# Kernel optimization log

Hardware: AMD Instinct MI355X
Metric: run time of the kernel (lower is better)

Reference implementation:

```python
import jax, jax.numpy as jnp
import numpy as np

H, N, D, K = 4, 512, 64, 64  # n_heads, node_num, d_model, sparse_k
TEMP = 0.5
EPS = 1e-10


def setup_inputs() -> dict:
    key = jax.random.key(0)
    k1, k2, k3 = jax.random.split(key, 3)
    feats = jax.random.normal(k1, (H, N, D), jnp.float32)
    # torch Linear init ~ U(-1/sqrt(fan_in), 1/sqrt(fan_in)); Gaussian scale is fine for a baseline
    W_out = jax.random.normal(k2, (2 * D, D), jnp.float32) * (1.0 / np.sqrt(2 * D))
    b_out = jnp.zeros((D,), jnp.float32)
    W_cat = jax.random.normal(k3, (D, 2), jnp.float32) * (1.0 / np.sqrt(D))
    b_cat = jnp.zeros((2,), jnp.float32)
    return {"feats": feats, "W_out": W_out, "b_out": b_out,
            "W_cat": W_cat, "b_cat": b_cat, "sparse_k": K}


def reference(feats, W_out, b_out, W_cat, b_cat, sparse_k):
    H_, N_, D_ = feats.shape
    E = N_ * N_
    e = jnp.arange(E)
    rec_idx = e // N_   # receiver node of edge e (rel_rec one-hot gather)
    snd_idx = e % N_    # sender node of edge e (rel_send one-hot gather)
    # cat([senders, receivers], -1): [H, E, 2D]
    x = jnp.concatenate([feats[:, snd_idx], feats[:, rec_idx]], axis=-1)
    h = jax.nn.relu(x @ W_out + b_out)          # [H, E, D]
    logits = h @ W_cat + b_cat                  # [H, E, 2]
    # gumbel-softmax, hard (straight-through)
    U = jax.random.uniform(jax.random.key(42), logits.shape, jnp.float32)
    g = -jnp.log(-jnp.log(U + EPS) + EPS)
    y_soft = jax.nn.softmax((logits + g) / TEMP, axis=-1)
    y_hard = jax.nn.one_hot(jnp.argmax(y_soft, axis=-1), 2, dtype=y_soft.dtype)
    y = jax.lax.stop_gradient(y_hard - y_soft) + y_soft
    connection_matrix = y[..., 1].reshape(H_, N_, N_)
    connection_prob = jax.nn.softmax(logits, axis=-1)[..., 1]  # [H, E]
    _, top_idx = jax.lax.top_k(connection_prob, sparse_k)      # top-k over edges per head
    sparse_labels = jnp.zeros_like(connection_prob).at[
        jnp.arange(H_)[:, None], top_idx].set(1.0)
    return connection_matrix, connection_prob, sparse_labels
```

## Files before the change

kernel.cpp:

```cpp
#include <hip/hip_runtime.h>
#include <stdint.h>

#define H_ 4
#define N_ 512
#define D_ 64
#define E_ (N_ * N_)
#define HE_ (H_ * E_)
#define EPS_ 1e-10f

__device__ __forceinline__ void tf2x32(unsigned x0, unsigned x1,
                                       unsigned& o0, unsigned& o1) {
  const unsigned ks0 = 0u;
  const unsigned ks1 = 42u;
  const unsigned ks2 = 0x1BD11BDAu ^ ks0 ^ ks1;
  x0 += ks0; x1 += ks1;
#define TFR(r) { x0 += x1; x1 = (x1 << (r)) | (x1 >> (32 - (r))); x1 ^= x0; }
  TFR(13) TFR(15) TFR(26) TFR(6)
  x0 += ks1; x1 += ks2 + 1u;
  TFR(17) TFR(29) TFR(16) TFR(24)
  x0 += ks2; x1 += ks0 + 2u;
  TFR(13) TFR(15) TFR(26) TFR(6)
  x0 += ks0; x1 += ks1 + 3u;
  TFR(17) TFR(29) TFR(16) TFR(24)
  x0 += ks1; x1 += ks2 + 4u;
  TFR(13) TFR(15) TFR(26) TFR(6)
  x0 += ks2; x1 += ks0 + 5u;
#undef TFR
  o0 = x0; o1 = x1;
}

__device__ __forceinline__ unsigned rng_bits(unsigned j) {
  unsigned a, b;
  tf2x32(0u, j, a, b);
  return a ^ b;
}

__device__ __forceinline__ float u01(unsigned bits) {
  return __uint_as_float((bits >> 9) | 0x3f800000u) - 1.0f;
}

__global__ __launch_bounds__(256) void precompute_ab(
    const float* __restrict__ feats, const float* __restrict__ W_out,
    float* __restrict__ A, float* __restrict__ B,
    unsigned* __restrict__ cnt, unsigned* __restrict__ done) {
  int row = blockIdx.x * 4 + (threadIdx.x >> 6);
  int d = threadIdx.x & 63;
  if (blockIdx.x == 0) {
    if (threadIdx.x < 4) cnt[threadIdx.x] = 0u;
    else if (threadIdx.x < 8) done[threadIdx.x - 4] = 0u;
  }
  __shared__ float f[4][64];
  f[threadIdx.x >> 6][d] = feats[row * D_ + d];
  __syncthreads();
  const float* fr = f[threadIdx.x >> 6];
  float a = 0.f, b = 0.f;
#pragma unroll 8
  for (int k = 0; k < D_; ++k) {
    float fv = fr[k];
    a = fmaf(fv, W_out[k * D_ + d], a);
    b = fmaf(fv, W_out[(k + D_) * D_ + d], b);
  }
  A[row * D_ + d] = a;
  B[row * D_ + d] = b;
}

__global__ __launch_bounds__(256, 4) void edge_kernel(
    const float* __restrict__ A, const float* __restrict__ B,
    const float* __restrict__ b_out, const float* __restrict__ W_cat,
    const float* __restrict__ b_cat, float* __restrict__ out,
    unsigned long long* __restrict__ blockmax) {
  __shared__ __align__(16) float Ash[64][68];
  __shared__ __align__(16) float Bsh[16][64];
  __shared__ float4 bsh4[16];
  __shared__ float4 wc4[32];
  __shared__ float bc2[2];
  __shared__ unsigned long long wmax[4];

  const int t = threadIdx.x;
  const int h = blockIdx.z;
  const int snd_base = blockIdx.x * 64;
  const int rec_base = blockIdx.y * 16;

  {
    const float4* A4 = (const float4*)(A + (h * N_ + snd_base) * D_);
    for (int i = t; i < 1024; i += 256)
      *(float4*)&Ash[i >> 4][(i & 15) << 2] = A4[i];
    const float4* B4 = (const float4*)(B + (h * N_ + rec_base) * D_);
    *(float4*)&Bsh[t >> 4][(t & 15) << 2] = B4[t];
  }
  if (t < 16) bsh4[t] = ((const float4*)b_out)[t];
  else if (t < 48) wc4[t - 16] = ((const float4*)W_cat)[t - 16];
  else if (t == 48) { bc2[0] = b_cat[0]; bc2[1] = b_cat[1]; }
  __syncthreads();

  const int s = t & 63;
  const int rg = (t >> 6) * 4;

  float l0[4], l1[4];
#pragma unroll
  for (int r = 0; r < 4; ++r) { l0[r] = 0.f; l1[r] = 0.f; }

#pragma unroll
  for (int d4 = 0; d4 < 16; ++d4) {
    const float4 a0 = *(const float4*)&Ash[s][d4 << 2];
    const float4 bd = bsh4[d4];
    const float4 wA = wc4[2 * d4];
    const float4 wB = wc4[2 * d4 + 1];
#pragma unroll
    for (int r = 0; r < 4; ++r) {
      const float4 bv = *(const float4*)&Bsh[rg + r][d4 << 2];
      float t0;
      t0 = fmaxf((a0.x + bv.x) + bd.x, 0.f);
      l0[r] = fmaf(t0, wA.x, l0[r]); l1[r] = fmaf(t0, wA.y, l1[r]);
      t0 = fmaxf((a0.y + bv.y) + bd.y, 0.f);
      l0[r] = fmaf(t0, wA.z, l0[r]); l1[r] = fmaf(t0, wA.w, l1[r]);
      t0 = fmaxf((a0.z + bv.z) + bd.z, 0.f);
      l0[r] = fmaf(t0, wB.x, l0[r]); l1[r] = fmaf(t0, wB.y, l1[r]);
      t0 = fmaxf((a0.w + bv.w) + bd.w, 0.f);
      l0[r] = fmaf(t0, wB.z, l0[r]); l1[r] = fmaf(t0, wB.w, l1[r]);
    }
  }

  unsigned long long mk = 0ull;
#pragma unroll
  for (int r = 0; r < 4; ++r) {
    float L0 = l0[r] + bc2[0];
    float L1 = l1[r] + bc2[1];
    const unsigned snd = (unsigned)(snd_base + s);
    const unsigned rec = (unsigned)(rec_base + rg + r);
    const unsigned e = rec * (unsigned)N_ + snd;
    const unsigned base = ((unsigned)h << 18) + e;
    const unsigned j0 = base * 2u;

    float uu0 = u01(rng_bits(j0));
    float uu1 = u01(rng_bits(j0 + 1u));
    float g0 = -logf(-logf(uu0 + EPS_) + EPS_);
    float g1 = -logf(-logf(uu1 + EPS_) + EPS_);

    float cm = ((L1 + g1) > (L0 + g0)) ? 1.0f : 0.0f;

    float lm = fmaxf(L0, L1);
    float p0 = expf(L0 - lm), p1 = expf(L1 - lm);
    float pr = p1 / (p0 + p1);

    out[base] = cm;
    out[HE_ + base] = pr;
    out[2 * HE_ + base] = 0.f;

    unsigned long long key =
        ((unsigned long long)__float_as_uint(pr) << 32) | (unsigned)(~e);
    mk = key > mk ? key : mk;
  }

#pragma unroll
  for (int off = 32; off; off >>= 1) {
    unsigned long long o = __shfl_xor(mk, off, 64);
    mk = o > mk ? o : mk;
  }
  if ((t & 63) == 0) wmax[t >> 6] = mk;
  __syncthreads();
  if (t == 0) {
    unsigned long long m = wmax[0];
#pragma unroll
    for (int i = 1; i < 4; ++i) m = wmax[i] > m ? wmax[i] : m;
    blockmax[h * 256 + blockIdx.y * gridDim.x + blockIdx.x] = m;
  }
}

__global__ __launch_bounds__(512) void topk_fused(
    const float* __restrict__ prob, const unsigned long long* __restrict__ blockmax,
    unsigned* __restrict__ cnt, unsigned* __restrict__ done,
    unsigned long long* __restrict__ cand, float* __restrict__ sparse) {
  __shared__ unsigned long long keys[512];
  __shared__ unsigned long long thrS;
  __shared__ unsigned tkS;
  const int t = threadIdx.x, h = blockIdx.y, blk = blockIdx.x;

  if (t < 256) keys[t] = blockmax[h * 256 + t];
  __syncthreads();
  if (t < 256) {
    unsigned long long my = keys[t];
    int rank = 0;
    for (int j = 0; j < 256; ++j) rank += (keys[j] > my);
    if (rank == 63) thrS = my;
  }
  __syncthreads();
  const unsigned long long thr = thrS;

  const unsigned seg = (unsigned)blk * 4096u;
#pragma unroll
  for (int i = 0; i < 2; ++i) {
    const unsigned e0 = seg + (unsigned)i * 2048u + (unsigned)t * 4u;
    float4 p = *(const float4*)(prob + (unsigned)h * E_ + e0);
    float pv[4] = {p.x, p.y, p.z, p.w};
#pragma unroll
    for (int k2 = 0; k2 < 4; ++k2) {
      unsigned e = e0 + (unsigned)k2;
      unsigned long long key =
          ((unsigned long long)__float_as_uint(pv[k2]) << 32) | (unsigned)(~e);
      if (key >= thr) {
        unsigned pos = atomicAdd(&cnt[h], 1u);
        if (pos < 512u) cand[h * 512 + pos] = key;
      }
    }
  }
  __syncthreads();
  if (t == 0) { __threadfence(); tkS = atomicAdd(&done[h], 1u); }
  __syncthreads();

  if (tkS == 63u) {
    if (t == 0) __threadfence();
    __syncthreads();
    unsigned n = atomicAdd(&cnt[h], 0u);
    if (n > 512u) n = 512u;
    keys[t] = (t < (int)n) ? cand[h * 512 + t] : 0ull;
    __syncthreads();
    for (int k = 2; k <= 512; k <<= 1)
      for (int j = k >> 1; j > 0; j >>= 1) {
        int ixj = t ^ j;
        if (ixj > t) {
          unsigned long long a = keys[t], b = keys[ixj];
          bool up = (t & k) == 0;
          if ((a > b) == up) { keys[t] = b; keys[ixj] = a; }
        }
        __syncthreads();
      }
    if (t >= 448) {
      unsigned e = ~(unsigned)(keys[t] & 0xFFFFFFFFull);
      if (e < (unsigned)E_) sparse[(unsigned)h * E_ + e] = 1.0f;
    }
  }
}

extern "C" void kernel_launch(void* const* d_in, const int* in_sizes, int n_in,
                              void* d_out, int out_size, void* d_ws, size_t ws_size,
                              hipStream_t stream) {
  const float* feats = (const float*)d_in[0];
  const float* W_out = (const float*)d_in[1];
  const float* b_out = (const float*)d_in[2];
  const float* W_cat = (const float*)d_in[3];
  const float* b_cat = (const float*)d_in[4];
  float* out = (float*)d_out;

  float* A = (float*)d_ws;
  float* B = A + H_ * N_ * D_;
  unsigned long long* blockmax = (unsigned long long*)(B + H_ * N_ * D_);
  unsigned long long* cand = blockmax + H_ * 256;
  unsigned* cnt = (unsigned*)(cand + H_ * 512);
  unsigned* done = cnt + H_;

  precompute_ab<<<dim3(H_ * N_ / 4), dim3(256), 0, stream>>>(feats, W_out, A, B,
                                                             cnt, done);
  edge_kernel<<<dim3(N_ / 64, N_ / 16, H_), dim3(256), 0, stream>>>(
      A, B, b_out, W_cat, b_cat, out, blockmax);
  topk_fused<<<dim3(64, H_), dim3(512), 0, stream>>>(out + HE_, blockmax, cnt,
                                                     done, cand, out + 2 * HE_);
}
```

Measured before the change: 107.8 us.

## Fuse top-k selection into edge kernel using a grid-wide spin barrier

Merges the edge and top-k kernels into one launch. Each block publishes its max key, spins on a per-head atomic counter until all 256 blocks of that head have arrived, computes the threshold, and pushes its register-held candidate keys directly. This avoids re-reading the probability array and one kernel launch. The sparse-label zeros are also written as float4 stores. The spin barrier assumes all 1024 blocks are co-resident (256 threads, up to 4 blocks per SIMD-bound launch); if they are not, it can deadlock.

```diff
diff --git a/kernel.cpp b/kernel.cpp
--- a/kernel.cpp
+++ b/kernel.cpp
@@ -41,14 +41,10 @@
 
 __global__ __launch_bounds__(256) void precompute_ab(
     const float* __restrict__ feats, const float* __restrict__ W_out,
-    float* __restrict__ A, float* __restrict__ B,
-    unsigned* __restrict__ cnt, unsigned* __restrict__ done) {
+    float* __restrict__ A, float* __restrict__ B, unsigned* __restrict__ ctrl) {
   int row = blockIdx.x * 4 + (threadIdx.x >> 6);
   int d = threadIdx.x & 63;
-  if (blockIdx.x == 0) {
-    if (threadIdx.x < 4) cnt[threadIdx.x] = 0u;
-    else if (threadIdx.x < 8) done[threadIdx.x - 4] = 0u;
-  }
+  if (blockIdx.x == 0 && threadIdx.x < 12) ctrl[threadIdx.x] = 0u;
   __shared__ float f[4][64];
   f[threadIdx.x >> 6][d] = feats[row * D_ + d];
   __syncthreads();
@@ -64,22 +60,29 @@
   B[row * D_ + d] = b;
 }
 
-__global__ __launch_bounds__(256, 4) void edge_kernel(
+__global__ __launch_bounds__(256, 4) void edge_topk(
     const float* __restrict__ A, const float* __restrict__ B,
     const float* __restrict__ b_out, const float* __restrict__ W_cat,
     const float* __restrict__ b_cat, float* __restrict__ out,
-    unsigned long long* __restrict__ blockmax) {
+    unsigned long long* __restrict__ blockmax,
+    unsigned long long* __restrict__ cand, unsigned* __restrict__ ctrl) {
   __shared__ __align__(16) float Ash[64][68];
   __shared__ __align__(16) float Bsh[16][64];
   __shared__ float4 bsh4[16];
   __shared__ float4 wc4[32];
   __shared__ float bc2[2];
   __shared__ unsigned long long wmax[4];
+  __shared__ unsigned long long sortk[512];
+  __shared__ unsigned long long thrS;
 
   const int t = threadIdx.x;
   const int h = blockIdx.z;
   const int snd_base = blockIdx.x * 64;
   const int rec_base = blockIdx.y * 16;
+  const int bm_idx = blockIdx.y * 8 + blockIdx.x;
+  unsigned* cnt = ctrl;
+  unsigned* done0 = ctrl + 4;
+  unsigned* done1 = ctrl + 8;
 
   {
     const float4* A4 = (const float4*)(A + (h * N_ + snd_base) * D_);
@@ -121,6 +124,7 @@
     }
   }
 
+  unsigned long long ekey[4];
   unsigned long long mk = 0ull;
 #pragma unroll
   for (int r = 0; r < 4; ++r) {
@@ -145,11 +149,18 @@
 
     out[base] = cm;
     out[HE_ + base] = pr;
-    out[2 * HE_ + base] = 0.f;
 
     unsigned long long key =
         ((unsigned long long)__float_as_uint(pr) << 32) | (unsigned)(~e);
+    ekey[r] = key;
     mk = key > mk ? key : mk;
+  }
+
+  {
+    const float4 z4 = {0.f, 0.f, 0.f, 0.f};
+    *(float4*)&out[2u * HE_ + ((unsigned)h << 18) +
+                   (unsigned)(rec_base + (t >> 4)) * N_ + (unsigned)snd_base +
+                   ((unsigned)(t & 15) << 2)] = z4;
   }
 
 #pragma unroll
@@ -160,74 +171,66 @@
   if ((t & 63) == 0) wmax[t >> 6] = mk;
   __syncthreads();
   if (t == 0) {
-    unsigned long long m = wmax[0];
-#pragma unroll
-    for (int i = 1; i < 4; ++i) m = wmax[i] > m ? wmax[i] : m;
-    blockmax[h * 256 + blockIdx.y * gridDim.x + blockIdx.x] = m;
-  }
-}
-
-__global__ __launch_bounds__(512) void topk_fused(
-    const float* __restrict__ prob, const unsigned long long* __restrict__ blockmax,
-    unsigned* __restrict__ cnt, unsigned* __restrict__ done,
-    unsigned long long* __restrict__ cand, float* __restrict__ sparse) {
-  __shared__ unsigned long long keys[512];
-  __shared__ unsigned long long thrS;
-  __shared__ unsigned tkS;
-  const int t = threadIdx.x, h = blockIdx.y, blk = blockIdx.x;
-
-  if (t < 256) keys[t] = blockmax[h * 256 + t];
-  __syncthreads();
-  if (t < 256) {
-    unsigned long long my = keys[t];
+    unsigned long long mx = wmax[0];
+#pragma unroll
+    for (int i = 1; i < 4; ++i) mx = wmax[i] > mx ? wmax[i] : mx;
+    blockmax[h * 256 + bm_idx] = mx;
+    __threadfence();
+    atomicAdd(&done0[h], 1u);
+    while (atomicAdd(&done0[h], 0u) < 256u) __builtin_amdgcn_s_sleep(2);
+    __threadfence();
+  }
+  __syncthreads();
+
+  sortk[t] = blockmax[h * 256 + t];
+  __syncthreads();
+  {
+    unsigned long long my = sortk[t];
     int rank = 0;
-    for (int j = 0; j < 256; ++j) rank += (keys[j] > my);
+    for (int j = 0; j < 256; ++j) rank += (sortk[j] > my);
     if (rank == 63) thrS = my;
   }
   __syncthreads();
   const unsigned long long thr = thrS;
 
-  const unsigned seg = (unsigned)blk * 4096u;
-#pragma unroll
-  for (int i = 0; i < 2; ++i) {
-    const unsigned e0 = seg + (unsigned)i * 2048u + (unsigned)t * 4u;
-    float4 p = *(const float4*)(prob + (unsigned)h * E_ + e0);
-    float pv[4] = {p.x, p.y, p.z, p.w};
-#pragma unroll
-    for (int k2 = 0; k2 < 4; ++k2) {
-      unsigned e = e0 + (unsigned)k2;
-      unsigned long long key =
-          ((unsigned long long)__float_as_uint(pv[k2]) << 32) | (unsigned)(~e);
-      if (key >= thr) {
-        unsigned pos = atomicAdd(&cnt[h], 1u);
-        if (pos < 512u) cand[h * 512 + pos] = key;
-      }
-    }
-  }
-  __syncthreads();
-  if (t == 0) { __threadfence(); tkS = atomicAdd(&done[h], 1u); }
-  __syncthreads();
-
-  if (tkS == 63u) {
-    if (t == 0) __threadfence();
+#pragma unroll
+  for (int r = 0; r < 4; ++r) {
+    if (ekey[r] >= thr) {
+      unsigned pos = atomicAdd(&cnt[h], 1u);
+      if (pos < 512u) cand[h * 512 + pos] = ekey[r];
+    }
+  }
+  __syncthreads();
+  if (t == 0) { __threadfence(); atomicAdd(&done1[h], 1u); }
+
+  if (bm_idx == 0) {
+    if (t == 0) {
+      while (atomicAdd(&done1[h], 0u) < 256u) __builtin_amdgcn_s_sleep(2);
+      __threadfence();
+    }
     __syncthreads();
     unsigned n = atomicAdd(&cnt[h], 0u);
     if (n > 512u) n = 512u;
-    keys[t] = (t < (int)n) ? cand[h * 512 + t] : 0ull;
+    sortk[t] = (t < (int)n) ? cand[h * 512 + t] : 0ull;
+    sortk[t + 256] = (t + 256 < (int)n) ? cand[h * 512 + t + 256] : 0ull;
     __syncthreads();
     for (int k = 2; k <= 512; k <<= 1)
       for (int j = k >> 1; j > 0; j >>= 1) {
-        int ixj = t ^ j;
-        if (ixj > t) {
-          unsigned long long a = keys[t], b = keys[ixj];
-          bool up = (t & k) == 0;
-          if ((a > b) == up) { keys[t] = b; keys[ixj] = a; }
+#pragma unroll
+        for (int half = 0; half < 2; ++half) {
+          int idx = t + half * 256;
+          int ixj = idx ^ j;
+          if (ixj > idx) {
+            unsigned long long x = sortk[idx], y = sortk[ixj];
+            bool up = (idx & k) == 0;
+            if ((x > y) == up) { sortk[idx] = y; sortk[ixj] = x; }
+          }
         }
         __syncthreads();
       }
-    if (t >= 448) {
-      unsigned e = ~(unsigned)(keys[t] & 0xFFFFFFFFull);
-      if (e < (unsigned)E_) sparse[(unsigned)h * E_ + e] = 1.0f;
+    if (t >= 192) {
+      unsigned e = ~(unsigned)(sortk[t + 256] & 0xFFFFFFFFull);
+      if (e < (unsigned)E_) out[2u * HE_ + ((unsigned)h << 18) + e] = 1.0f;
     }
   }
 }
@@ -246,13 +249,10 @@
   float* B = A + H_ * N_ * D_;
   unsigned long long* blockmax = (unsigned long long*)(B + H_ * N_ * D_);
   unsigned long long* cand = blockmax + H_ * 256;
-  unsigned* cnt = (unsigned*)(cand + H_ * 512);
-  unsigned* done = cnt + H_;
+  unsigned* ctrl = (unsigned*)(cand + H_ * 512);
 
   precompute_ab<<<dim3(H_ * N_ / 4), dim3(256), 0, stream>>>(feats, W_out, A, B,
-                                                             cnt, done);
-  edge_kernel<<<dim3(N_ / 64, N_ / 16, H_), dim3(256), 0, stream>>>(
-      A, B, b_out, W_cat, b_cat, out, blockmax);
-  topk_fused<<<dim3(64, H_), dim3(512), 0, stream>>>(out + HE_, blockmax, cnt,
-                                                     done, cand, out + 2 * HE_);
-}
+                                                             ctrl);
+  edge_topk<<<dim3(N_ / 64, N_ / 16, H_), dim3(256), 0, stream>>>(
+      A, B, b_out, W_cat, b_cat, out, blockmax, cand, ctrl);
+}
```

Measured after the change: 222.1 us. 2.06x slower.
